# Performance work log

Measured on AMD Instinct MI355X. Metric: run time of the kernel, lower is better.

## Reference

```python
import jax, jax.numpy as jnp
import numpy as np

N, E, D, H = 50000, 500000, 128, 8
DH = D // H  # per-head dim = int(out_dim // num_heads)
EPS_LN = 1e-5
EPS_BN = 1e-5


def _ln(x, g, b):
    m = x.mean(-1, keepdims=True)
    v = ((x - m) ** 2).mean(-1, keepdims=True)
    return (x - m) * jax.lax.rsqrt(v + EPS_LN) * g + b


def _bn(x, g, b):
    # BatchNorm1d, training-mode statistics (biased variance over the batch)
    m = x.mean(0)
    v = ((x - m) ** 2).mean(0)
    return (x - m) * jax.lax.rsqrt(v + EPS_BN) * g + b


def setup_inputs() -> dict:
    key = jax.random.key(0)
    ks = jax.random.split(key, 16)
    rn = lambda k, shape: (jax.random.normal(k, shape, jnp.float32) * 0.05)
    h = jax.random.normal(ks[0], (N, D), jnp.float32)
    src = jax.random.randint(ks[1], (E,), 0, N).astype(jnp.int32)
    # guarantee every node receives at least one message so z > 0 (no 0/0)
    dst = jnp.concatenate([jnp.arange(N, dtype=jnp.int32),
                           jax.random.randint(ks[2], (E - N,), 0, N).astype(jnp.int32)])
    return {
        "h": h, "src": src, "dst": dst,
        # per-node TransformerEncoder (seq_len == 1 subgraphs)
        "Win": rn(ks[3], (3 * D, D)), "bin": jnp.zeros((3 * D,), jnp.float32),
        "Wout": rn(ks[4], (D, D)), "bout": jnp.zeros((D,), jnp.float32),
        "Wte1": rn(ks[5], (4 * D, D)), "bte1": jnp.zeros((4 * D,), jnp.float32),
        "Wte2": rn(ks[6], (D, 4 * D)), "bte2": jnp.zeros((D,), jnp.float32),
        "ln1g": jnp.ones((D,), jnp.float32), "ln1b": jnp.zeros((D,), jnp.float32),
        "ln2g": jnp.ones((D,), jnp.float32), "ln2b": jnp.zeros((D,), jnp.float32),
        # graph multi-head attention projections (use_bias=False)
        "WQ": rn(ks[7], (D, D)), "WK": rn(ks[8], (D, D)), "WV": rn(ks[9], (D, D)),
        # node-wise FFN + batch norms
        "W1": rn(ks[10], (2 * D, D)), "b1": jnp.zeros((2 * D,), jnp.float32),
        "W2": rn(ks[11], (D, 2 * D)), "b2": jnp.zeros((D,), jnp.float32),
        "bn1g": jnp.ones((D,), jnp.float32), "bn1b": jnp.zeros((D,), jnp.float32),
        "bn2g": jnp.ones((D,), jnp.float32), "bn2b": jnp.zeros((D,), jnp.float32),
    }


def _forward(h, src, dst, Win, bin_, Wout, bout, Wte1, bte1, Wte2, bte2,
             ln1g, ln1b, ln2g, ln2b, WQ, WK, WV,
             W1, b1, W2, b2, bn1g, bn1b, bn2g, bn2b):
    # --- per-node TransformerEncoder. Each dgl.node_subgraph(g, [i]) contains
    # only the center node, so self-attention runs over a length-1 sequence:
    # softmax of a single score is 1, hence attn_out = out_proj(v).
    v = h @ Win[2 * D:].T + bin_[2 * D:]            # V slice of in_proj
    x = _ln(h + (v @ Wout.T + bout), ln1g, ln1b)
    ff = jax.nn.relu(x @ Wte1.T + bte1) @ Wte2.T + bte2
    hsub = _ln(x + ff, ln2g, ln2b)                  # [N, D]

    # --- graph multi-head attention (DGL apply_edges / send_and_recv)
    Qh = (hsub @ WQ.T).reshape(N, H, DH)
    Kh = (hsub @ WK.T).reshape(N, H, DH)
    Vh = (hsub @ WV.T).reshape(N, H, DH)
    score = (Kh[src] * Qh[dst]).sum(-1)             # [E, H]  K_src . Q_dst
    score = jnp.exp(jnp.clip(score / np.sqrt(DH), -5.0, 5.0))
    wV = jax.ops.segment_sum(Vh[src] * score[:, :, None], dst, num_segments=N)
    z = jax.ops.segment_sum(score, dst, num_segments=N)
    attn = (wV / z[:, :, None]).reshape(N, D)

    # --- residual + BN + FFN + residual + BN (dropout p=0 / eval mode)
    hh = _bn(hsub + attn, bn1g, bn1b)
    h_in2 = hh
    hh = jax.nn.relu(hh @ W1.T + b1) @ W2.T + b2
    return _bn(h_in2 + hh, bn2g, bn2b)


def reference(h, src, dst, Win, bin, Wout, bout, Wte1, bte1, Wte2, bte2,
              ln1g, ln1b, ln2g, ln2b, WQ, WK, WV,
              W1, b1, W2, b2, bn1g, bn1b, bn2g, bn2b):
    return _forward(h, src, dst, Win, bin, Wout, bout, Wte1, bte1, Wte2, bte2,
                    ln1g, ln1b, ln2g, ln2b, WQ, WK, WV,
                    W1, b1, W2, b2, bn1g, bn1b, bn2g, bn2b)
```

## Files before the change

kernel.cpp:

```cpp
#include <hip/hip_runtime.h>
#include <hip/hip_bf16.h>


#define D_ 128

typedef __attribute__((ext_vector_type(8))) short short8;
typedef __attribute__((ext_vector_type(4))) short short4v;
typedef __attribute__((ext_vector_type(4))) float f32x4;

__device__ __forceinline__ float b2f(ushort u) {
    union { uint u32; float f; } x; x.u32 = ((uint)u) << 16; return x.f;
}
__device__ __forceinline__ ushort f2b(float f) {
    union { __hip_bfloat16 h; ushort u; } v; v.h = __float2bfloat16(f); return v.u;
}

template<int AMODE, int EPI, bool RELU, bool RESF32>
__global__ __launch_bounds__(512) void gemm_bf16(
    const void* __restrict__ Aptr, const ushort* __restrict__ W,
    const float* __restrict__ bias, void* __restrict__ C,
    const float* __restrict__ bn_in, float* __restrict__ bn_out,
    const float* __restrict__ bng, const float* __restrict__ bnb,
    const void* __restrict__ resid, const ushort* __restrict__ y1res,
    const float* __restrict__ lng, const float* __restrict__ lnb,
    float invn, int n, int K, int M)
{
    __shared__ ushort Abuf[2][128 * 32];
    __shared__ ushort Bbuf[2][128 * 32];
    __shared__ float s_sh[128], t_sh[128];

    const int t    = threadIdx.x;
    const int lane = t & 63;
    const int w    = t >> 6;
    const int r0   = blockIdx.x * 128;
    const int c0   = blockIdx.y * 128;
    const int wr   = (w >> 1) * 32;
    const int wc   = (w & 1) * 64;
    const int rl   = lane & 15;
    const int kh   = lane >> 4;

    if (AMODE == 2 || EPI == 2) {
        if (t < 128) {
            float m   = bn_in[t] * invn;
            float var = bn_in[128 + t] * invn - m * m;
            float rs  = rsqrtf(var + 1e-5f);
            float s   = rs * bng[t];
            s_sh[t] = s;
            t_sh[t] = bnb[t] - m * s;
        }
        __syncthreads();
    }

    f32x4 acc[2][4] = {};
    const int nc = K >> 5;
    const int row = t >> 2, pos = t & 3;

    if (AMODE == 1) {
        for (int c = 0; c < nc; ++c) {
            int kc = c * 32;
            const int ch = pos;
            int gr = r0 + row;
            short8 aval = {};
            if (gr < n) {
                const float* Af = (const float*)Aptr;
                float4 f0 = *reinterpret_cast<const float4*>(Af + (size_t)gr * K + kc + ch * 8);
                float4 f1 = *reinterpret_cast<const float4*>(Af + (size_t)gr * K + kc + ch * 8 + 4);
                aval[0] = (short)f2b(f0.x); aval[1] = (short)f2b(f0.y);
                aval[2] = (short)f2b(f0.z); aval[3] = (short)f2b(f0.w);
                aval[4] = (short)f2b(f1.x); aval[5] = (short)f2b(f1.y);
                aval[6] = (short)f2b(f1.z); aval[7] = (short)f2b(f1.w);
            }
            short8 bval = *reinterpret_cast<const short8*>(W + (size_t)(c0 + row) * K + kc + ch * 8);
            __syncthreads();
            int sw = ch ^ ((row >> 1) & 3);
            *reinterpret_cast<short8*>(&Abuf[0][row * 32 + sw * 8]) = aval;
            *reinterpret_cast<short8*>(&Bbuf[0][row * 32 + sw * 8]) = bval;
            __syncthreads();
            short8 af[2], bfr[4];
            #pragma unroll
            for (int m = 0; m < 2; ++m) {
                int rr = wr + m * 16 + rl;
                af[m] = *reinterpret_cast<const short8*>(&Abuf[0][rr * 32 + (kh ^ ((rr >> 1) & 3)) * 8]);
            }
            #pragma unroll
            for (int nn = 0; nn < 4; ++nn) {
                int col = wc + nn * 16 + rl;
                bfr[nn] = *reinterpret_cast<const short8*>(&Bbuf[0][col * 32 + (kh ^ ((col >> 1) & 3)) * 8]);
            }
            #pragma unroll
            for (int m = 0; m < 2; ++m)
                #pragma unroll
                for (int nn = 0; nn < 4; ++nn)
                    acc[m][nn] = __builtin_amdgcn_mfma_f32_16x16x32_bf16(
                        bfr[nn], af[m], acc[m][nn], 0, 0, 0);
        }
    } else {
        const int ch = pos ^ ((row >> 1) & 3);
        const ushort* Abase = (const ushort*)Aptr + (size_t)(r0 + row) * K + ch * 8;
        const ushort* Bbase = W + (size_t)(c0 + row) * K + ch * 8;
        __builtin_amdgcn_global_load_lds(
            (const __attribute__((address_space(1))) void*)Abase,
            (__attribute__((address_space(3))) void*)&Abuf[0][t * 8], 16, 0, 0);
        __builtin_amdgcn_global_load_lds(
            (const __attribute__((address_space(1))) void*)Bbase,
            (__attribute__((address_space(3))) void*)&Bbuf[0][t * 8], 16, 0, 0);
        __syncthreads();
        for (int c = 0; c < nc; ++c) {
            if (c + 1 < nc) {
                int half = (c + 1) & 1;
                __builtin_amdgcn_global_load_lds(
                    (const __attribute__((address_space(1))) void*)(Abase + (c + 1) * 32),
                    (__attribute__((address_space(3))) void*)&Abuf[half][t * 8], 16, 0, 0);
                __builtin_amdgcn_global_load_lds(
                    (const __attribute__((address_space(1))) void*)(Bbase + (c + 1) * 32),
                    (__attribute__((address_space(3))) void*)&Bbuf[half][t * 8], 16, 0, 0);
            }
            const int cur = c & 1;
            const int kc  = c * 32;
            short8 af[2], bfr[4];
            #pragma unroll
            for (int m = 0; m < 2; ++m) {
                int rr = wr + m * 16 + rl;
                af[m] = *reinterpret_cast<const short8*>(&Abuf[cur][rr * 32 + (kh ^ ((rr >> 1) & 3)) * 8]);
            }
            if (AMODE == 2) {
                #pragma unroll
                for (int m = 0; m < 2; ++m) {
                    short8 v = af[m];
                    #pragma unroll
                    for (int q = 0; q < 8; ++q) {
                        int cch = kc + kh * 8 + q;
                        v[q] = (short)f2b(fmaf(b2f((ushort)v[q]), s_sh[cch], t_sh[cch]));
                    }
                    af[m] = v;
                }
            }
            #pragma unroll
            for (int nn = 0; nn < 4; ++nn) {
                int col = wc + nn * 16 + rl;
                bfr[nn] = *reinterpret_cast<const short8*>(&Bbuf[cur][col * 32 + (kh ^ ((col >> 1) & 3)) * 8]);
            }
            #pragma unroll
            for (int m = 0; m < 2; ++m)
                #pragma unroll
                for (int nn = 0; nn < 4; ++nn)
                    acc[m][nn] = __builtin_amdgcn_mfma_f32_16x16x32_bf16(
                        bfr[nn], af[m], acc[m][nn], 0, 0, 0);
            __syncthreads();
        }
    }

    const int ch4 = kh * 4;

    if (EPI == 1) {
        __shared__ float lnS[128][2], lnS2[128][2];
        float4 bb[4];
        #pragma unroll
        for (int nn = 0; nn < 4; ++nn)
            bb[nn] = *reinterpret_cast<const float4*>(bias + wc + nn * 16 + ch4);
        #pragma unroll
        for (int m = 0; m < 2; ++m) {
            int r = r0 + wr + m * 16 + rl;
            float s = 0.f, s2 = 0.f;
            #pragma unroll
            for (int nn = 0; nn < 4; ++nn) {
                int c = wc + nn * 16 + ch4;
                float rv[4] = {0.f, 0.f, 0.f, 0.f};
                if (r < n) {
                    if (RESF32) {
                        float4 f = *reinterpret_cast<const float4*>((const float*)resid + (size_t)r * 128 + c);
                        rv[0] = f.x; rv[1] = f.y; rv[2] = f.z; rv[3] = f.w;
                    } else {
                        short4v f = *reinterpret_cast<const short4v*>((const ushort*)resid + (size_t)r * 128 + c);
                        rv[0] = b2f((ushort)f[0]); rv[1] = b2f((ushort)f[1]);
                        rv[2] = b2f((ushort)f[2]); rv[3] = b2f((ushort)f[3]);
                    }
                }
                float bj[4] = {bb[nn].x, bb[nn].y, bb[nn].z, bb[nn].w};
                #pragma unroll
                for (int j = 0; j < 4; ++j) {
                    float o = acc[m][nn][j] + bj[j] + rv[j];
                    acc[m][nn][j] = o;
                    s += o; s2 += o * o;
                }
            }
            s  += __shfl_xor(s, 16);  s  += __shfl_xor(s, 32);
            s2 += __shfl_xor(s2, 16); s2 += __shfl_xor(s2, 32);
            if (kh == 0) {
                lnS[wr + m * 16 + rl][w & 1]  = s;
                lnS2[wr + m * 16 + rl][w & 1] = s2;
            }
        }
        __syncthreads();
        #pragma unroll
        for (int m = 0; m < 2; ++m) {
            int rloc = wr + m * 16 + rl;
            int r = r0 + rloc;
            float S  = lnS[rloc][0] + lnS[rloc][1];
            float S2 = lnS2[rloc][0] + lnS2[rloc][1];
            float mean = S * (1.f / 128.f);
            float var  = S2 * (1.f / 128.f) - mean * mean;
            float rs   = rsqrtf(var + 1e-5f);
            if (r >= n) continue;
            #pragma unroll
            for (int nn = 0; nn < 4; ++nn) {
                int c = wc + nn * 16 + ch4;
                float4 gv = *reinterpret_cast<const float4*>(lng + c);
                float4 bv = *reinterpret_cast<const float4*>(lnb + c);
                float gj[4] = {gv.x, gv.y, gv.z, gv.w};
                float bj[4] = {bv.x, bv.y, bv.z, bv.w};
                short4v p;
                #pragma unroll
                for (int j = 0; j < 4; ++j)
                    p[j] = (short)f2b((acc[m][nn][j] - mean) * rs * gj[j] + bj[j]);
                *reinterpret_cast<short4v*>((ushort*)C + (size_t)r * 128 + c) = p;
            }
        }
        return;
    }

    if (EPI == 2) {
        __shared__ float csum[128], csum2[128];
        if (t < 128) { csum[t] = 0.f; csum2[t] = 0.f; }
        __syncthreads();
        float ps[4][4] = {};
        float ps2[4][4] = {};
        #pragma unroll
        for (int m = 0; m < 2; ++m) {
            int r = r0 + wr + m * 16 + rl;
            bool ok = r < n;
            #pragma unroll
            for (int nn = 0; nn < 4; ++nn) {
                int c = wc + nn * 16 + ch4;
                float4 bb = *reinterpret_cast<const float4*>(bias + c);
                float bj[4] = {bb.x, bb.y, bb.z, bb.w};
                short4v yv = {};
                if (ok) yv = *reinterpret_cast<const short4v*>(y1res + (size_t)r * 128 + c);
                short4v p;
                #pragma unroll
                for (int j = 0; j < 4; ++j) {
                    float o = 0.f;
                    if (ok) {
                        o = acc[m][nn][j] + bj[j]
                          + fmaf(b2f((ushort)yv[j]), s_sh[c + j], t_sh[c + j]);
                    }
                    ps[nn][j] += o; ps2[nn][j] += o * o;
                    p[j] = (short)f2b(o);
                }
                if (ok)
                    *reinterpret_cast<short4v*>((ushort*)C + (size_t)r * 128 + c) = p;
            }
        }
        #pragma unroll
        for (int nn = 0; nn < 4; ++nn)
            #pragma unroll
            for (int j = 0; j < 4; ++j) {
                float a = ps[nn][j], b = ps2[nn][j];
                #pragma unroll
                for (int o2 = 1; o2 < 16; o2 <<= 1) {
                    a += __shfl_xor(a, o2);
                    b += __shfl_xor(b, o2);
                }
                if (rl == 0) {
                    int c = wc + nn * 16 + ch4 + j;
                    atomicAdd(&csum[c], a);
                    atomicAdd(&csum2[c], b);
                }
            }
        __syncthreads();
        if (t < 128) {
            atomicAdd(bn_out + t, csum[t]);
            atomicAdd(bn_out + 128 + t, csum2[t]);
        }
        return;
    }

    #pragma unroll
    for (int m = 0; m < 2; ++m) {
        int r = r0 + wr + m * 16 + rl;
        if (r >= n) continue;
        #pragma unroll
        for (int nn = 0; nn < 4; ++nn) {
            int c = c0 + wc + nn * 16 + ch4;
            f32x4 vacc = acc[m][nn];
            float4 bb = make_float4(0.f, 0.f, 0.f, 0.f);
            if (bias) bb = *reinterpret_cast<const float4*>(bias + c);
            float o0 = vacc[0] + bb.x, o1 = vacc[1] + bb.y;
            float o2 = vacc[2] + bb.z, o3 = vacc[3] + bb.w;
            if (RELU) {
                o0 = fmaxf(o0, 0.f); o1 = fmaxf(o1, 0.f);
                o2 = fmaxf(o2, 0.f); o3 = fmaxf(o3, 0.f);
            }
            short4v p;
            p[0] = (short)f2b(o0); p[1] = (short)f2b(o1);
            p[2] = (short)f2b(o2); p[3] = (short)f2b(o3);
            *reinterpret_cast<short4v*>((ushort*)C + (size_t)r * M + c) = p;
        }
    }
}

__global__ __launch_bounds__(512) void ffn_ln_kernel(
    const ushort* __restrict__ X,   const ushort* __restrict__ W1g,
    const ushort* __restrict__ W2g,
    const float* __restrict__ b1v,  const float* __restrict__ b2v,
    const float* __restrict__ lng,  const float* __restrict__ lnb,
    ushort* __restrict__ out, int n)
{
    __shared__ ushort Xs[128 * 128];
    __shared__ ushort FF1[128 * 64];
    __shared__ ushort W1s[64 * 128];
    __shared__ ushort W2s[128 * 64];

    const int t    = threadIdx.x;
    const int lane = t & 63;
    const int w    = t >> 6;
    const int r0   = blockIdx.x * 128;
    const int rl   = lane & 15;
    const int kh   = lane >> 4;
    const int wr   = (w >> 1) * 32;
    const int wc1  = (w & 1) * 32;
    const int wc2  = (w & 1) * 64;

    #pragma unroll
    for (int i = 0; i < 4; ++i) {
        int s = t + i * 512;
        int row = s >> 4, pos = s & 15;
        int srcch = pos ^ ((row >> 1) & 7);
        if (r0 + row < n)
            __builtin_amdgcn_global_load_lds(
                (const __attribute__((address_space(1))) void*)(X + (size_t)(r0 + row) * 128 + srcch * 8),
                (__attribute__((address_space(3))) void*)&Xs[s * 8], 16, 0, 0);
    }
    __syncthreads();

    f32x4 acc2[2][4] = {};

    for (int c = 0; c < 8; ++c) {
        #pragma unroll
        for (int i = 0; i < 2; ++i) {
            int s = t + i * 512;
            int row = s >> 4, pos = s & 15;
            int srcch = pos ^ ((row >> 1) & 7);
            __builtin_amdgcn_global_load_lds(
                (const __attribute__((address_space(1))) void*)(W1g + (size_t)(c * 64 + row) * 128 + srcch * 8),
                (__attribute__((address_space(3))) void*)&W1s[s * 8], 16, 0, 0);
        }
        #pragma unroll
        for (int i = 0; i < 2; ++i) {
            int s = t + i * 512;
            int row = s >> 3, pos = s & 7;
            int srcch = pos ^ ((row >> 1) & 7);
            __builtin_amdgcn_global_load_lds(
                (const __attribute__((address_space(1))) void*)(W2g + (size_t)row * 512 + c * 64 + srcch * 8),
                (__attribute__((address_space(3))) void*)&W2s[s * 8], 16, 0, 0);
        }
        __syncthreads();

        f32x4 acc1[2][2] = {};
        #pragma unroll
        for (int ks = 0; ks < 4; ++ks) {
            short8 af[2], bf[2];
            #pragma unroll
            for (int m = 0; m < 2; ++m) {
                int row = wr + m * 16 + rl;
                int chn = ks * 4 + kh;
                af[m] = *reinterpret_cast<const short8*>(&Xs[row * 128 + (chn ^ ((row >> 1) & 7)) * 8]);
            }
            #pragma unroll
            for (int nn = 0; nn < 2; ++nn) {
                int colL = wc1 + nn * 16 + rl;
                int chn = ks * 4 + kh;
                bf[nn] = *reinterpret_cast<const short8*>(&W1s[colL * 128 + (chn ^ ((colL >> 1) & 7)) * 8]);
            }
            #pragma unroll
            for (int m = 0; m < 2; ++m)
                #pragma unroll
                for (int nn = 0; nn < 2; ++nn)
                    acc1[m][nn] = __builtin_amdgcn_mfma_f32_16x16x32_bf16(
                        bf[nn], af[m], acc1[m][nn], 0, 0, 0);
        }
        #pragma unroll
        for (int m = 0; m < 2; ++m) {
            int row = wr + m * 16 + rl;
            #pragma unroll
            for (int nn = 0; nn < 2; ++nn) {
                int colL = wc1 + nn * 16 + kh * 4;
                float4 bb = *reinterpret_cast<const float4*>(b1v + c * 64 + colL);
                short4v p;
                p[0] = (short)f2b(fmaxf(acc1[m][nn][0] + bb.x, 0.f));
                p[1] = (short)f2b(fmaxf(acc1[m][nn][1] + bb.y, 0.f));
                p[2] = (short)f2b(fmaxf(acc1[m][nn][2] + bb.z, 0.f));
                p[3] = (short)f2b(fmaxf(acc1[m][nn][3] + bb.w, 0.f));
                int chn = colL >> 3, half = (colL >> 2) & 1;
                *reinterpret_cast<short4v*>(
                    &FF1[row * 64 + (chn ^ ((row >> 1) & 7)) * 8 + half * 4]) = p;
            }
        }
        __syncthreads();

        #pragma unroll
        for (int ks = 0; ks < 2; ++ks) {
            short8 af[2], bf[4];
            #pragma unroll
            for (int m = 0; m < 2; ++m) {
                int row = wr + m * 16 + rl;
                int chn = ks * 4 + kh;
                af[m] = *reinterpret_cast<const short8*>(&FF1[row * 64 + (chn ^ ((row >> 1) & 7)) * 8]);
            }
            #pragma unroll
            for (int nn = 0; nn < 4; ++nn) {
                int col = wc2 + nn * 16 + rl;
                int chn = ks * 4 + kh;
                bf[nn] = *reinterpret_cast<const short8*>(&W2s[col * 64 + (chn ^ ((col >> 1) & 7)) * 8]);
            }
            #pragma unroll
            for (int m = 0; m < 2; ++m)
                #pragma unroll
                for (int nn = 0; nn < 4; ++nn)
                    acc2[m][nn] = __builtin_amdgcn_mfma_f32_16x16x32_bf16(
                        bf[nn], af[m], acc2[m][nn], 0, 0, 0);
        }
        __syncthreads();
    }

    float* lnSf  = (float*)FF1;
    float* lnS2f = lnSf + 256;
    const int ch4 = kh * 4;
    #pragma unroll
    for (int m = 0; m < 2; ++m) {
        int rloc = wr + m * 16 + rl;
        float s = 0.f, s2 = 0.f;
        #pragma unroll
        for (int nn = 0; nn < 4; ++nn) {
            int col = wc2 + nn * 16 + ch4;
            int chn = col >> 3;
            short4v xv = *reinterpret_cast<const short4v*>(
                &Xs[rloc * 128 + (chn ^ ((rloc >> 1) & 7)) * 8 + ((col >> 2) & 1) * 4]);
            float4 bb = *reinterpret_cast<const float4*>(b2v + col);
            float bj[4] = {bb.x, bb.y, bb.z, bb.w};
            #pragma unroll
            for (int j = 0; j < 4; ++j) {
                float o = acc2[m][nn][j] + bj[j] + b2f((ushort)xv[j]);
                acc2[m][nn][j] = o;
                s += o; s2 += o * o;
            }
        }
        s  += __shfl_xor(s, 16);  s  += __shfl_xor(s, 32);
        s2 += __shfl_xor(s2, 16); s2 += __shfl_xor(s2, 32);
        if (kh == 0) {
            lnSf[rloc * 2 + (w & 1)]  = s;
            lnS2f[rloc * 2 + (w & 1)] = s2;
        }
    }
    __syncthreads();
    #pragma unroll
    for (int m = 0; m < 2; ++m) {
        int rloc = wr + m * 16 + rl;
        int r = r0 + rloc;
        float S  = lnSf[rloc * 2 + 0] + lnSf[rloc * 2 + 1];
        float S2 = lnS2f[rloc * 2 + 0] + lnS2f[rloc * 2 + 1];
        float mean = S * (1.f / 128.f);
        float var  = S2 * (1.f / 128.f) - mean * mean;
        float rs   = rsqrtf(var + 1e-5f);
        if (r >= n) continue;
        #pragma unroll
        for (int nn = 0; nn < 4; ++nn) {
            int col = wc2 + nn * 16 + ch4;
            float4 gv = *reinterpret_cast<const float4*>(lng + col);
            float4 bv = *reinterpret_cast<const float4*>(lnb + col);
            float gj[4] = {gv.x, gv.y, gv.z, gv.w};
            float bj[4] = {bv.x, bv.y, bv.z, bv.w};
            short4v p;
            #pragma unroll
            for (int j = 0; j < 4; ++j)
                p[j] = (short)f2b((acc2[m][nn][j] - mean) * rs * gj[j] + bj[j]);
            *reinterpret_cast<short4v*>(out + (size_t)r * 128 + col) = p;
        }
    }
}

__global__ __launch_bounds__(256) void zero_kernel(int4* __restrict__ p, int n4)
{
    int i = blockIdx.x * blockDim.x + threadIdx.x;
    int stride = gridDim.x * blockDim.x;
    int4 z = make_int4(0, 0, 0, 0);
    for (; i < n4; i += stride) p[i] = z;
}

__global__ void hist_kernel(const int* __restrict__ dst, int* __restrict__ cnt, int E_)
{
    int e = blockIdx.x * blockDim.x + threadIdx.x;
    if (e < E_) atomicAdd(cnt + dst[e], 1);
}

__global__ __launch_bounds__(256) void scan_block_kernel(
    int* __restrict__ data, int* __restrict__ bsum, int n)
{
    __shared__ int tmp[256];
    int i = blockIdx.x * 256 + threadIdx.x;
    int v = (i < n) ? data[i] : 0;
    tmp[threadIdx.x] = v;
    __syncthreads();
    #pragma unroll
    for (int o = 1; o < 256; o <<= 1) {
        int y = (threadIdx.x >= o) ? tmp[threadIdx.x - o] : 0;
        __syncthreads();
        tmp[threadIdx.x] += y;
        __syncthreads();
    }
    if (i < n) data[i] = tmp[threadIdx.x] - v;
    if (threadIdx.x == 255) bsum[blockIdx.x] = tmp[255];
}

__global__ __launch_bounds__(256) void add_off_kernel(
    int* __restrict__ data, const int* __restrict__ bsum, int n, int nb)
{
    __shared__ int red[4];
    int b = blockIdx.x;
    int v = (threadIdx.x < b && threadIdx.x < nb) ? bsum[threadIdx.x] : 0;
    #pragma unroll
    for (int o = 1; o < 64; o <<= 1) v += __shfl_xor(v, o);
    if ((threadIdx.x & 63) == 0) red[threadIdx.x >> 6] = v;
    __syncthreads();
    int off = red[0] + red[1] + red[2] + red[3];
    int i = b * 256 + threadIdx.x;
    if (i < n) data[i] += off;
}

__global__ void scatter_kernel(const int* __restrict__ src, const int* __restrict__ dst,
                               int* __restrict__ rowptr, int* __restrict__ csr_src, int E_)
{
    int e = blockIdx.x * blockDim.x + threadIdx.x;
    if (e >= E_) return;
    int pos = atomicAdd(rowptr + dst[e], 1);
    csr_src[pos] = src[e];
}

__global__ __launch_bounds__(256) void attn_agg_kernel(
    const int* __restrict__ rowptr, const int* __restrict__ csr_src,
    const ushort* __restrict__ QKV, const ushort* __restrict__ hsub,
    ushort* __restrict__ out, int n)
{
    int node  = (blockIdx.x * blockDim.x + threadIdx.x) >> 5;
    int lane5 = threadIdx.x & 31;
    int slot  = lane5 >> 3;
    int hd    = lane5 & 7;
    bool valid = node < n;
    int nd = valid ? node : 0;
    int start = (valid && nd) ? rowptr[nd - 1] : 0;
    int end   = valid ? rowptr[nd] : 0;

    const ushort* qp = QKV + (size_t)nd * 384 + hd * 16;
    short8 q0 = *reinterpret_cast<const short8*>(qp);
    short8 q1 = *reinterpret_cast<const short8*>(qp + 8);
    float q[16];
    #pragma unroll
    for (int i = 0; i < 8; ++i) { q[i] = b2f((ushort)q0[i]); q[8 + i] = b2f((ushort)q1[i]); }

    float acc[16] = {};
    float zh = 0.f;
    for (int j = start; j < end; j += 4) {
        int idx = j + slot;
        if (idx < end) {
            int s = csr_src[idx];
            const ushort* kp = QKV + (size_t)s * 384 + 128 + hd * 16;
            short8 k0 = *reinterpret_cast<const short8*>(kp);
            short8 k1 = *reinterpret_cast<const short8*>(kp + 8);
            float p = 0.f;
            #pragma unroll
            for (int i = 0; i < 8; ++i) {
                p = fmaf(b2f((ushort)k0[i]), q[i], p);
                p = fmaf(b2f((ushort)k1[i]), q[8 + i], p);
            }
            float sc = __expf(fminf(fmaxf(p * 0.25f, -5.f), 5.f));
            short8 v0 = *reinterpret_cast<const short8*>(kp + 128);
            short8 v1 = *reinterpret_cast<const short8*>(kp + 136);
            #pragma unroll
            for (int i = 0; i < 8; ++i) {
                acc[i]     = fmaf(sc, b2f((ushort)v0[i]), acc[i]);
                acc[8 + i] = fmaf(sc, b2f((ushort)v1[i]), acc[8 + i]);
            }
            zh += sc;
        }
    }
    #pragma unroll
    for (int i = 0; i < 16; ++i) {
        acc[i] += __shfl_xor(acc[i], 8);
        acc[i] += __shfl_xor(acc[i], 16);
    }
    zh += __shfl_xor(zh, 8);
    zh += __shfl_xor(zh, 16);

    if (slot == 0 && valid) {
        const ushort* hp = hsub + (size_t)nd * D_ + hd * 16;
        short8 h0 = *reinterpret_cast<const short8*>(hp);
        short8 h1 = *reinterpret_cast<const short8*>(hp + 8);
        float inv = 1.f / zh;
        short8 o0, o1;
        #pragma unroll
        for (int i = 0; i < 8; ++i) {
            o0[i] = (short)f2b(b2f((ushort)h0[i]) + acc[i] * inv);
            o1[i] = (short)f2b(b2f((ushort)h1[i]) + acc[8 + i] * inv);
        }
        ushort* op = out + (size_t)nd * D_ + hd * 16;
        *reinterpret_cast<short8*>(op)     = o0;
        *reinterpret_cast<short8*>(op + 8) = o1;
    }
}

__global__ __launch_bounds__(256) void bn_stats_kernel(
    const ushort* __restrict__ x, float* __restrict__ sums, int n)
{
    int c    = threadIdx.x & 127;
    int half = threadIdx.x >> 7;
    float s = 0.f, s2 = 0.f;
    for (int r = blockIdx.x * 2 + half; r < n; r += gridDim.x * 2) {
        float v = b2f(x[(size_t)r * D_ + c]);
        s += v; s2 += v * v;
    }
    __shared__ float ls[256], ls2[256];
    ls[threadIdx.x] = s; ls2[threadIdx.x] = s2;
    __syncthreads();
    if (half == 0) {
        s  += ls[threadIdx.x + 128];
        s2 += ls2[threadIdx.x + 128];
        atomicAdd(sums + c, s);
        atomicAdd(sums + 128 + c, s2);
    }
}

__global__ void bn_norm_kernel(const ushort* __restrict__ x,
                               const float* __restrict__ stats,
                               const float* __restrict__ g, const float* __restrict__ b,
                               float* __restrict__ out, float invn, int total4)
{
    int i = blockIdx.x * blockDim.x + threadIdx.x;
    if (i >= total4) return;
    int cb = (i << 2) & 127;
    short4v v = reinterpret_cast<const short4v*>(x)[i];
    float4 o;
    float r[4];
    #pragma unroll
    for (int q = 0; q < 4; ++q) {
        int c = cb + q;
        float m   = stats[c] * invn;
        float var = stats[128 + c] * invn - m * m;
        float rs  = rsqrtf(var + 1e-5f);
        r[q] = (b2f((ushort)v[q]) - m) * rs * g[c] + b[c];
    }
    o.x = r[0]; o.y = r[1]; o.z = r[2]; o.w = r[3];
    reinterpret_cast<float4*>(out)[i] = o;
}

struct WPtrs { const float* p[7]; };

__global__ __launch_bounds__(256) void prep_w_kernel(
    const float* __restrict__ Win, const float* __restrict__ bin_,
    const float* __restrict__ Wout, const float* __restrict__ bout,
    WPtrs wp, ushort* __restrict__ wbf, float* __restrict__ bfused)
{
    int b = blockIdx.x;
    if (b < 64) {
        int idx = b * 256 + threadIdx.x;
        int i = idx >> 7, c = idx & 127;
        const float* WinV = Win + 256 * 128;
        float s = 0.f;
        for (int j = 0; j < 128; ++j)
            s = fmaf(Wout[i * 128 + j], WinV[j * 128 + c], s);
        wbf[245760 + idx] = f2b(s);
        if (c == 0) {
            float tb = bout[i];
            for (int j = 0; j < 128; ++j)
                tb = fmaf(Wout[i * 128 + j], bin_[256 + j], tb);
            bfused[i] = tb;
        }
    } else {
        const int off[8] = {0, 65536, 131072, 147456, 163840, 180224, 212992, 245760};
        int e0 = ((b - 64) * 256 + threadIdx.x) * 4;
        if (e0 >= 245760) return;
        int s = 0;
        #pragma unroll
        for (int j = 1; j < 7; ++j) if (e0 >= off[j]) s = j;
        float4 f = *reinterpret_cast<const float4*>(wp.p[s] + (e0 - off[s]));
        short4v o;
        o[0] = (short)f2b(f.x); o[1] = (short)f2b(f.y);
        o[2] = (short)f2b(f.z); o[3] = (short)f2b(f.w);
        *reinterpret_cast<short4v*>(wbf + e0) = o;
    }
}

extern "C" void kernel_launch(void* const* d_in, const int* in_sizes, int n_in,
                              void* d_out, int out_size, void* d_ws, size_t ws_size,
                              hipStream_t stream)
{
    const float* h    = (const float*)d_in[0];
    const int*   src  = (const int*)d_in[1];
    const int*   dst  = (const int*)d_in[2];
    const float* Win  = (const float*)d_in[3];
    const float* bin_ = (const float*)d_in[4];
    const float* Wout = (const float*)d_in[5];
    const float* bout = (const float*)d_in[6];
    const float* Wte1 = (const float*)d_in[7];
    const float* bte1 = (const float*)d_in[8];
    const float* Wte2 = (const float*)d_in[9];
    const float* bte2 = (const float*)d_in[10];
    const float* ln1g = (const float*)d_in[11];
    const float* ln1b = (const float*)d_in[12];
    const float* ln2g = (const float*)d_in[13];
    const float* ln2b = (const float*)d_in[14];
    const float* WQ   = (const float*)d_in[15];
    const float* WK   = (const float*)d_in[16];
    const float* WV   = (const float*)d_in[17];
    const float* W1   = (const float*)d_in[18];
    const float* b1   = (const float*)d_in[19];
    const float* W2   = (const float*)d_in[20];
    const float* b2   = (const float*)d_in[21];
    const float* bn1g = (const float*)d_in[22];
    const float* bn1b = (const float*)d_in[23];
    const float* bn2g = (const float*)d_in[24];
    const float* bn2b = (const float*)d_in[25];

    const int N_ = in_sizes[0] / D_;
    const int E_ = in_sizes[1];
    const size_t S2 = (size_t)N_ * D_ / 2;

    float* ws = (float*)d_ws;
    size_t off_tail = 7 * S2;
    size_t need = (off_tail + 131072 + 128 + 512) * sizeof(float)
                + (size_t)(N_ + E_ + 256) * sizeof(int) + 4096;
    if (ws_size < need) return;

    ushort* bufA   = (ushort*)ws;
    ushort* bufB   = (ushort*)(ws + S2);
    ushort* bufC   = (ushort*)(ws + 2 * S2);
    ushort* bufD   = (ushort*)(ws + 3 * S2);
    ushort* wbf    = (ushort*)(ws + off_tail);
    float*  bfused = ws + off_tail + 131072;
    float*  stats  = bfused + 128;
    int* rowptr  = (int*)(stats + 512);
    int* csr_src = rowptr + N_;
    int* bsum    = csr_src + E_;

    const ushort* Wte1_bf = wbf;
    const ushort* Wte2_bf = wbf + 65536;
    const ushort* WQKV_bf = wbf + 131072;
    const ushort* W1_bf   = wbf + 180224;
    const ushort* W2_bf   = wbf + 212992;
    ushort*       Wf_bf   = wbf + 245760;

    dim3 blk(256);
    dim3 blk512(512);
    const int rowBlocks = (N_ + 127) / 128;
    const int totElems  = N_ * D_;
    const dim3 gNode((N_ + 7) / 8);
    const int nb = (N_ + 255) / 256;
    const float invn = 1.f / (float)N_;

    {
        int n4 = (512 + N_) / 4;
        int zblocks = (n4 + 255) / 256;
        if (zblocks > 128) zblocks = 128;
        zero_kernel<<<dim3(zblocks), blk, 0, stream>>>((int4*)stats, n4);
    }

    hist_kernel<<<dim3((E_ + 255) / 256), blk, 0, stream>>>(dst, rowptr, E_);
    scan_block_kernel<<<dim3(nb), blk, 0, stream>>>(rowptr, bsum, N_);
    add_off_kernel<<<dim3(nb), blk, 0, stream>>>(rowptr, bsum, N_, nb);
    scatter_kernel<<<dim3((E_ + 255) / 256), blk, 0, stream>>>(src, dst, rowptr, csr_src, E_);

    WPtrs wp;
    wp.p[0] = Wte1; wp.p[1] = Wte2; wp.p[2] = WQ; wp.p[3] = WK; wp.p[4] = WV;
    wp.p[5] = W1;   wp.p[6] = W2;
    prep_w_kernel<<<dim3(304), blk, 0, stream>>>(Win, bin_, Wout, bout, wp, wbf, bfused);

    gemm_bf16<1, 1, false, true><<<dim3(rowBlocks, 1), blk512, 0, stream>>>(
        h, Wf_bf, bfused, bufA, nullptr, nullptr, nullptr, nullptr,
        h, nullptr, ln1g, ln1b, 0.f, N_, 128, 128);
    ffn_ln_kernel<<<dim3(rowBlocks), blk512, 0, stream>>>(
        bufA, Wte1_bf, Wte2_bf, bte1, bte2, ln2g, ln2b, bufC, N_);

    gemm_bf16<0, 0, false, false><<<dim3(rowBlocks, 3), blk512, 0, stream>>>(
        bufC, WQKV_bf, nullptr, bufD, nullptr, nullptr, nullptr, nullptr,
        nullptr, nullptr, nullptr, nullptr, 0.f, N_, 128, 384);
    attn_agg_kernel<<<gNode, blk, 0, stream>>>(
        rowptr, csr_src, bufD, bufC, bufA, N_);

    bn_stats_kernel<<<dim3(512), blk, 0, stream>>>(bufA, stats, N_);

    gemm_bf16<2, 0, true, false><<<dim3(rowBlocks, 2), blk512, 0, stream>>>(
        bufA, W1_bf, b1, bufD, stats, nullptr, bn1g, bn1b,
        nullptr, nullptr, nullptr, nullptr, invn, N_, 128, 256);
    gemm_bf16<0, 2, false, false><<<dim3(rowBlocks, 1), blk512, 0, stream>>>(
        bufD, W2_bf, b2, bufB, stats, stats + 256, bn1g, bn1b,
        nullptr, bufA, nullptr, nullptr, invn, N_, 256, 128);
    bn_norm_kernel<<<dim3((totElems / 4 + 255) / 256), blk, 0, stream>>>(
        bufB, stats + 256, bn2g, bn2b, (float*)d_out, invn, totElems / 4);
}
```

Baseline: 252.7 us.

## Keep post-attention residual stream in fp32 and widen attention aggregation to 64 lanes

```diff
diff --git a/kernel.cpp b/kernel.cpp
--- a/kernel.cpp
+++ b/kernel.cpp
@@ -21,7 +21,7 @@
     const float* __restrict__ bias, void* __restrict__ C,
     const float* __restrict__ bn_in, float* __restrict__ bn_out,
     const float* __restrict__ bng, const float* __restrict__ bnb,
-    const void* __restrict__ resid, const ushort* __restrict__ y1res,
+    const void* __restrict__ resid, const float* __restrict__ y1res,
     const float* __restrict__ lng, const float* __restrict__ lnb,
     float invn, int n, int K, int M)
 {
@@ -39,7 +39,7 @@
     const int rl   = lane & 15;
     const int kh   = lane >> 4;
 
-    if (AMODE == 2 || EPI == 2) {
+    if (AMODE == 3 || EPI == 2) {
         if (t < 128) {
             float m   = bn_in[t] * invn;
             float var = bn_in[128 + t] * invn - m * m;
@@ -55,7 +55,7 @@
     const int nc = K >> 5;
     const int row = t >> 2, pos = t & 3;
 
-    if (AMODE == 1) {
+    if (AMODE == 1 || AMODE == 3) {
         for (int c = 0; c < nc; ++c) {
             int kc = c * 32;
             const int ch = pos;
@@ -65,10 +65,16 @@
                 const float* Af = (const float*)Aptr;
                 float4 f0 = *reinterpret_cast<const float4*>(Af + (size_t)gr * K + kc + ch * 8);
                 float4 f1 = *reinterpret_cast<const float4*>(Af + (size_t)gr * K + kc + ch * 8 + 4);
-                aval[0] = (short)f2b(f0.x); aval[1] = (short)f2b(f0.y);
-                aval[2] = (short)f2b(f0.z); aval[3] = (short)f2b(f0.w);
-                aval[4] = (short)f2b(f1.x); aval[5] = (short)f2b(f1.y);
-                aval[6] = (short)f2b(f1.z); aval[7] = (short)f2b(f1.w);
+                float fv[8] = {f0.x, f0.y, f0.z, f0.w, f1.x, f1.y, f1.z, f1.w};
+                #pragma unroll
+                for (int q = 0; q < 8; ++q) {
+                    float v = fv[q];
+                    if (AMODE == 3) {
+                        int cch = kc + ch * 8 + q;
+                        v = fmaf(v, s_sh[cch], t_sh[cch]);
+                    }
+                    aval[q] = (short)f2b(v);
+                }
             }
             short8 bval = *reinterpret_cast<const short8*>(W + (size_t)(c0 + row) * K + kc + ch * 8);
             __syncthreads();
@@ -116,24 +122,11 @@
                     (__attribute__((address_space(3))) void*)&Bbuf[half][t * 8], 16, 0, 0);
             }
             const int cur = c & 1;
-            const int kc  = c * 32;
             short8 af[2], bfr[4];
             #pragma unroll
             for (int m = 0; m < 2; ++m) {
                 int rr = wr + m * 16 + rl;
                 af[m] = *reinterpret_cast<const short8*>(&Abuf[cur][rr * 32 + (kh ^ ((rr >> 1) & 3)) * 8]);
-            }
-            if (AMODE == 2) {
-                #pragma unroll
-                for (int m = 0; m < 2; ++m) {
-                    short8 v = af[m];
-                    #pragma unroll
-                    for (int q = 0; q < 8; ++q) {
-                        int cch = kc + kh * 8 + q;
-                        v[q] = (short)f2b(fmaf(b2f((ushort)v[q]), s_sh[cch], t_sh[cch]));
-                    }
-                    af[m] = v;
-                }
             }
             #pragma unroll
             for (int nn = 0; nn < 4; ++nn) {
@@ -234,21 +227,24 @@
                 int c = wc + nn * 16 + ch4;
                 float4 bb = *reinterpret_cast<const float4*>(bias + c);
                 float bj[4] = {bb.x, bb.y, bb.z, bb.w};
-                short4v yv = {};
-                if (ok) yv = *reinterpret_cast<const short4v*>(y1res + (size_t)r * 128 + c);
-                short4v p;
+                float4 yv = make_float4(0.f, 0.f, 0.f, 0.f);
+                if (ok) yv = *reinterpret_cast<const float4*>(y1res + (size_t)r * 128 + c);
+                float yj[4] = {yv.x, yv.y, yv.z, yv.w};
+                float oj[4];
                 #pragma unroll
                 for (int j = 0; j < 4; ++j) {
                     float o = 0.f;
                     if (ok) {
                         o = acc[m][nn][j] + bj[j]
-                          + fmaf(b2f((ushort)yv[j]), s_sh[c + j], t_sh[c + j]);
+                          + fmaf(yj[j], s_sh[c + j], t_sh[c + j]);
                     }
                     ps[nn][j] += o; ps2[nn][j] += o * o;
-                    p[j] = (short)f2b(o);
+                    oj[j] = o;
                 }
-                if (ok)
-                    *reinterpret_cast<short4v*>((ushort*)C + (size_t)r * 128 + c) = p;
+                if (ok) {
+                    float4 o4 = make_float4(oj[0], oj[1], oj[2], oj[3]);
+                    *reinterpret_cast<float4*>((float*)C + (size_t)r * 128 + c) = o4;
+                }
             }
         }
         #pragma unroll
@@ -539,18 +535,17 @@
 __global__ __launch_bounds__(256) void attn_agg_kernel(
     const int* __restrict__ rowptr, const int* __restrict__ csr_src,
     const ushort* __restrict__ QKV, const ushort* __restrict__ hsub,
-    ushort* __restrict__ out, int n)
-{
-    int node  = (blockIdx.x * blockDim.x + threadIdx.x) >> 5;
-    int lane5 = threadIdx.x & 31;
-    int slot  = lane5 >> 3;
-    int hd    = lane5 & 7;
-    bool valid = node < n;
-    int nd = valid ? node : 0;
-    int start = (valid && nd) ? rowptr[nd - 1] : 0;
-    int end   = valid ? rowptr[nd] : 0;
-
-    const ushort* qp = QKV + (size_t)nd * 384 + hd * 16;
+    float* __restrict__ out, int n)
+{
+    int node = (blockIdx.x * blockDim.x + threadIdx.x) >> 6;
+    if (node >= n) return;
+    int lane = threadIdx.x & 63;
+    int slot = lane >> 3;
+    int hd   = lane & 7;
+    int start = node ? rowptr[node - 1] : 0;
+    int end   = rowptr[node];
+
+    const ushort* qp = QKV + (size_t)node * 384 + hd * 16;
     short8 q0 = *reinterpret_cast<const short8*>(qp);
     short8 q1 = *reinterpret_cast<const short8*>(qp + 8);
     float q[16];
@@ -559,7 +554,7 @@
 
     float acc[16] = {};
     float zh = 0.f;
-    for (int j = start; j < end; j += 4) {
+    for (int j = start; j < end; j += 8) {
         int idx = j + slot;
         if (idx < end) {
             int s = csr_src[idx];
@@ -587,35 +582,50 @@
     for (int i = 0; i < 16; ++i) {
         acc[i] += __shfl_xor(acc[i], 8);
         acc[i] += __shfl_xor(acc[i], 16);
+        acc[i] += __shfl_xor(acc[i], 32);
     }
     zh += __shfl_xor(zh, 8);
     zh += __shfl_xor(zh, 16);
-
-    if (slot == 0 && valid) {
-        const ushort* hp = hsub + (size_t)nd * D_ + hd * 16;
+    zh += __shfl_xor(zh, 32);
+
+    if (slot == 0) {
+        const ushort* hp = hsub + (size_t)node * D_ + hd * 16;
         short8 h0 = *reinterpret_cast<const short8*>(hp);
         short8 h1 = *reinterpret_cast<const short8*>(hp + 8);
         float inv = 1.f / zh;
-        short8 o0, o1;
-        #pragma unroll
-        for (int i = 0; i < 8; ++i) {
-            o0[i] = (short)f2b(b2f((ushort)h0[i]) + acc[i] * inv);
-            o1[i] = (short)f2b(b2f((ushort)h1[i]) + acc[8 + i] * inv);
-        }
-        ushort* op = out + (size_t)nd * D_ + hd * 16;
-        *reinterpret_cast<short8*>(op)     = o0;
-        *reinterpret_cast<short8*>(op + 8) = o1;
+        float* op = out + (size_t)node * D_ + hd * 16;
+        float4 o;
+        o.x = b2f((ushort)h0[0]) + acc[0] * inv;
+        o.y = b2f((ushort)h0[1]) + acc[1] * inv;
+        o.z = b2f((ushort)h0[2]) + acc[2] * inv;
+        o.w = b2f((ushort)h0[3]) + acc[3] * inv;
+        reinterpret_cast<float4*>(op)[0] = o;
+        o.x = b2f((ushort)h0[4]) + acc[4] * inv;
+        o.y = b2f((ushort)h0[5]) + acc[5] * inv;
+        o.z = b2f((ushort)h0[6]) + acc[6] * inv;
+        o.w = b2f((ushort)h0[7]) + acc[7] * inv;
+        reinterpret_cast<float4*>(op)[1] = o;
+        o.x = b2f((ushort)h1[0]) + acc[8]  * inv;
+        o.y = b2f((ushort)h1[1]) + acc[9]  * inv;
+        o.z = b2f((ushort)h1[2]) + acc[10] * inv;
+        o.w = b2f((ushort)h1[3]) + acc[11] * inv;
+        reinterpret_cast<float4*>(op)[2] = o;
+        o.x = b2f((ushort)h1[4]) + acc[12] * inv;
+        o.y = b2f((ushort)h1[5]) + acc[13] * inv;
+        o.z = b2f((ushort)h1[6]) + acc[14] * inv;
+        o.w = b2f((ushort)h1[7]) + acc[15] * inv;
+        reinterpret_cast<float4*>(op)[3] = o;
     }
 }
 
 __global__ __launch_bounds__(256) void bn_stats_kernel(
-    const ushort* __restrict__ x, float* __restrict__ sums, int n)
+    const float* __restrict__ x, float* __restrict__ sums, int n)
 {
     int c    = threadIdx.x & 127;
     int half = threadIdx.x >> 7;
     float s = 0.f, s2 = 0.f;
     for (int r = blockIdx.x * 2 + half; r < n; r += gridDim.x * 2) {
-        float v = b2f(x[(size_t)r * D_ + c]);
+        float v = x[(size_t)r * D_ + c];
         s += v; s2 += v * v;
     }
     __shared__ float ls[256], ls2[256];
@@ -629,7 +639,7 @@
     }
 }
 
-__global__ void bn_norm_kernel(const ushort* __restrict__ x,
+__global__ void bn_norm_kernel(const float* __restrict__ x,
                                const float* __restrict__ stats,
                                const float* __restrict__ g, const float* __restrict__ b,
                                float* __restrict__ out, float invn, int total4)
@@ -637,8 +647,8 @@
     int i = blockIdx.x * blockDim.x + threadIdx.x;
     if (i >= total4) return;
     int cb = (i << 2) & 127;
-    short4v v = reinterpret_cast<const short4v*>(x)[i];
-    float4 o;
+    float4 v = reinterpret_cast<const float4*>(x)[i];
+    float vj[4] = {v.x, v.y, v.z, v.w};
     float r[4];
     #pragma unroll
     for (int q = 0; q < 4; ++q) {
@@ -646,9 +656,9 @@
         float m   = stats[c] * invn;
         float var = stats[128 + c] * invn - m * m;
         float rs  = rsqrtf(var + 1e-5f);
-        r[q] = (b2f((ushort)v[q]) - m) * rs * g[c] + b[c];
-    }
-    o.x = r[0]; o.y = r[1]; o.z = r[2]; o.w = r[3];
+        r[q] = (vj[q] - m) * rs * g[c] + b[c];
+    }
+    float4 o; o.x = r[0]; o.y = r[1]; o.z = r[2]; o.w = r[3];
     reinterpret_cast<float4*>(out)[i] = o;
 }
 
@@ -725,15 +735,16 @@
     const size_t S2 = (size_t)N_ * D_ / 2;
 
     float* ws = (float*)d_ws;
-    size_t off_tail = 7 * S2;
+    size_t off_tail = 10 * S2;
     size_t need = (off_tail + 131072 + 128 + 512) * sizeof(float)
                 + (size_t)(N_ + E_ + 256) * sizeof(int) + 4096;
     if (ws_size < need) return;
 
     ushort* bufA   = (ushort*)ws;
-    ushort* bufB   = (ushort*)(ws + S2);
-    ushort* bufC   = (ushort*)(ws + 2 * S2);
-    ushort* bufD   = (ushort*)(ws + 3 * S2);
+    ushort* bufC   = (ushort*)(ws + S2);
+    ushort* bufD   = (ushort*)(ws + 2 * S2);
+    float*  y1f    = ws + 6 * S2;
+    float*  y2f    = ws + 8 * S2;
     ushort* wbf    = (ushort*)(ws + off_tail);
     float*  bfused = ws + off_tail + 131072;
     float*  stats  = bfused + 128;
@@ -752,7 +763,7 @@
     dim3 blk512(512);
     const int rowBlocks = (N_ + 127) / 128;
     const int totElems  = N_ * D_;
-    const dim3 gNode((N_ + 7) / 8);
+    const dim3 gNode((N_ + 3) / 4);
     const int nb = (N_ + 255) / 256;
     const float invn = 1.f / (float)N_;
 
@@ -783,16 +794,16 @@
         bufC, WQKV_bf, nullptr, bufD, nullptr, nullptr, nullptr, nullptr,
         nullptr, nullptr, nullptr, nullptr, 0.f, N_, 128, 384);
     attn_agg_kernel<<<gNode, blk, 0, stream>>>(
-        rowptr, csr_src, bufD, bufC, bufA, N_);
-
-    bn_stats_kernel<<<dim3(512), blk, 0, stream>>>(bufA, stats, N_);
-
-    gemm_bf16<2, 0, true, false><<<dim3(rowBlocks, 2), blk512, 0, stream>>>(
-        bufA, W1_bf, b1, bufD, stats, nullptr, bn1g, bn1b,
+        rowptr, csr_src, bufD, bufC, y1f, N_);
+
+    bn_stats_kernel<<<dim3(512), blk, 0, stream>>>(y1f, stats, N_);
+
+    gemm_bf16<3, 0, true, false><<<dim3(rowBlocks, 2), blk512, 0, stream>>>(
+        y1f, W1_bf, b1, bufD, stats, nullptr, bn1g, bn1b,
         nullptr, nullptr, nullptr, nullptr, invn, N_, 128, 256);
     gemm_bf16<0, 2, false, false><<<dim3(rowBlocks, 1), blk512, 0, stream>>>(
-        bufD, W2_bf, b2, bufB, stats, stats + 256, bn1g, bn1b,
-        nullptr, bufA, nullptr, nullptr, invn, N_, 256, 128);
+        bufD, W2_bf, b2, y2f, stats, stats + 256, bn1g, bn1b,
+        nullptr, y1f, nullptr, nullptr, invn, N_, 256, 128);
     bn_norm_kernel<<<dim3((totElems / 4 + 255) / 256), blk, 0, stream>>>(
-        bufB, stats + 256, bn2g, bn2b, (float*)d_out, invn, totElems / 4);
-}
+        y2f, stats + 256, bn2g, bn2b, (float*)d_out, invn, totElems / 4);
+}
```

Result: slower. 260.6 us (+3.1%).
